# Kernel optimization log

Hardware: AMD Instinct MI355X
Metric: run time of the kernel (lower is better)

Reference implementation:

```python
import jax, jax.numpy as jnp
import numpy as np

N, E, EQ = 100000, 600000, 200000
F_IN, HID, N_CONVS = 128, 128, 4  # n_layers=3 -> 4 conv blocks
BN_EPS = 1e-5


def setup_inputs() -> dict:
    key = jax.random.key(0)
    ks = jax.random.split(key, 16)
    s = 1.0 / np.sqrt(HID)
    inp = {
        "x": jax.random.normal(ks[0], (N, F_IN), jnp.float32),
        "edge_index": jax.random.randint(ks[1], (2, E), 0, N, jnp.int64),
        "edge_attr": jax.random.uniform(ks[2], (E,), jnp.float32),
        "edge_label_index": jax.random.randint(ks[3], (2, EQ), 0, N, jnp.int64),
        # GraphConv params (layer 0 has in_dim == hidden_dim, so stack all 4)
        "rel_w": jax.random.normal(ks[4], (N_CONVS, HID, HID), jnp.float32) * s,
        "rel_b": jnp.zeros((N_CONVS, HID), jnp.float32),
        "root_w": jax.random.normal(ks[5], (N_CONVS, HID, HID), jnp.float32) * s,
        "bn_g": jnp.ones((N_CONVS, HID), jnp.float32),
        "bn_b": jnp.zeros((N_CONVS, HID), jnp.float32),
        # edge MLP: Linear(2H->H), GELU, Linear(H->1)
        "mlp_w1": jax.random.normal(ks[6], (2 * HID, HID), jnp.float32) * (1.0 / np.sqrt(2 * HID)),
        "mlp_b1": jnp.zeros((HID,), jnp.float32),
        "mlp_w2": jax.random.normal(ks[7], (HID, 1), jnp.float32) * s,
        "mlp_b2": jnp.zeros((1,), jnp.float32),
    }
    return inp


def reference(x, edge_index, edge_attr, edge_label_index,
              rel_w, rel_b, root_w, bn_g, bn_b,
              mlp_w1, mlp_b1, mlp_w2, mlp_b2):
    src, dst = edge_index[0], edge_index[1]
    n = x.shape[0]
    for l in range(rel_w.shape[0]):
        # GraphConv: lin_rel(sum_j w_ij * x_j) + lin_root(x_i)
        msg = x[src] * edge_attr[:, None]                      # [E, H] gather
        agg = jax.ops.segment_sum(msg, dst, num_segments=n)    # [N, H] scatter-add
        h = agg @ rel_w[l] + rel_b[l] + x @ root_w[l]
        h = jax.nn.gelu(h, approximate=False)
        # BatchNorm over nodes (training-mode batch stats, biased var)
        mean = h.mean(axis=0)
        var = h.var(axis=0)
        x = (h - mean) * jax.lax.rsqrt(var + BN_EPS) * bn_g[l] + bn_b[l]
    ef = jnp.concatenate([x[edge_label_index[0]], x[edge_label_index[1]]], axis=-1)  # [EQ, 2H]
    hmid = jax.nn.gelu(ef @ mlp_w1 + mlp_b1, approximate=False)
    out = jax.nn.sigmoid(hmid @ mlp_w2 + mlp_b2)
    return out.squeeze(-1)
```

## Files before the change

kernel.cpp:

```cpp
#include <hip/hip_runtime.h>

#define NN 100000
#define EE 600000
#define NQ 200000
#define HID 128
#define NL 4
#define BN_EPS 1e-5f
#define ECAP 1280

typedef __attribute__((ext_vector_type(8))) short short8;
typedef __attribute__((ext_vector_type(4))) float f32x4;

__device__ __forceinline__ float gelu_f(float v) {
    return 0.5f * v * (1.0f + erff(v * 0.70710678118654752f));
}
__device__ __forceinline__ unsigned short f2bf(float f) {
    unsigned int x = __float_as_uint(f);
    unsigned int r = (x + 0x7FFFu + ((x >> 16) & 1u)) >> 16;
    return (unsigned short)r;
}
__device__ __forceinline__ float bf2f(unsigned short u) {
    return __uint_as_float(((unsigned int)u) << 16);
}


__global__ void k_zero_int(int* __restrict__ p, int n) {
    int i = blockIdx.x * blockDim.x + threadIdx.x;
    if (i < n) p[i] = 0;
}

__global__ void k_cvt(const float* __restrict__ x, unsigned int* __restrict__ o, int n2) {
    int i = blockIdx.x * blockDim.x + threadIdx.x;
    if (i < n2) {
        float2 v = ((const float2*)x)[i];
        o[i] = (unsigned int)f2bf(v.x) | ((unsigned int)f2bf(v.y) << 16);
    }
}

__global__ void k_bninit(float* __restrict__ sc) {
    int i = threadIdx.x;
    sc[i] = (i < 128) ? 1.0f : 0.0f;
}


__global__ void k_hist(const int* __restrict__ ei, int* __restrict__ cnt) {
    int e = blockIdx.x * blockDim.x + threadIdx.x;
    if (e < EE) atomicAdd(&cnt[ei[EE + e]], 1);
}

__global__ void k_scan1(const int* __restrict__ cnt, int* __restrict__ rp,
                        int* __restrict__ bsum, int n) {
    __shared__ int sh[256];
    const int tid = threadIdx.x;
    const int base = blockIdx.x * 1024;
    int v[4];
    int s = 0;
    #pragma unroll
    for (int j = 0; j < 4; ++j) {
        int idx = base + tid * 4 + j;
        v[j] = (idx < n) ? cnt[idx] : 0;
        s += v[j];
    }
    sh[tid] = s;
    __syncthreads();
    for (int off = 1; off < 256; off <<= 1) {
        int t = (tid >= off) ? sh[tid - off] : 0;
        __syncthreads();
        sh[tid] += t;
        __syncthreads();
    }
    int run = sh[tid] - s;
    #pragma unroll
    for (int j = 0; j < 4; ++j) {
        int idx = base + tid * 4 + j;
        if (idx < n) rp[idx] = run;
        run += v[j];
    }
    if (tid == 255) bsum[blockIdx.x] = sh[255];
}

__global__ void k_scan2(int* __restrict__ bsum, int nb) {
    __shared__ int sh[256];
    const int tid = threadIdx.x;
    int v = (tid < nb) ? bsum[tid] : 0;
    sh[tid] = v;
    __syncthreads();
    for (int off = 1; off < 256; off <<= 1) {
        int t = (tid >= off) ? sh[tid - off] : 0;
        __syncthreads();
        sh[tid] += t;
        __syncthreads();
    }
    if (tid < nb) bsum[tid] = sh[tid] - v;
}

__global__ void k_scan3(int* __restrict__ rp, const int* __restrict__ bsum,
                        int* __restrict__ cnt, int n) {
    int i = blockIdx.x * blockDim.x + threadIdx.x;
    if (i < n) {
        rp[i] += bsum[i >> 10];
        cnt[i] = 0;
    }
    if (i == 0) rp[n] = EE;
}

__global__ void k_fill(const int* __restrict__ ei, const int* __restrict__ rp,
                       int* __restrict__ cur, int* __restrict__ eord) {
    int e = blockIdx.x * blockDim.x + threadIdx.x;
    if (e < EE) {
        int d = ei[EE + e];
        int p = rp[d] + atomicAdd(&cur[d], 1);
        eord[p] = e;
    }
}

__global__ void k_sortfill(const int* __restrict__ ei, const float* __restrict__ ea,
                           const int* __restrict__ rp, int* __restrict__ eord,
                           int* __restrict__ csrc, float* __restrict__ cea,
                           float* __restrict__ wdeg) {
    int n = blockIdx.x * blockDim.x + threadIdx.x;
    if (n >= NN) return;
    const int s0 = rp[n], s1 = rp[n + 1];
    for (int i = s0 + 1; i < s1; ++i) {
        int key = eord[i];
        int j = i - 1;
        while (j >= s0 && eord[j] > key) { eord[j + 1] = eord[j]; --j; }
        eord[j + 1] = key;
    }
    float s = 0.f;
    for (int i = s0; i < s1; ++i) {
        const int e = eord[i];
        csrc[i] = ei[e];
        const float w = ea[e];
        cea[i] = w;
        s += w;
    }
    wdeg[n] = s;
}


__global__ void k_wprep(const float* __restrict__ relw, const float* __restrict__ rootw,
                        const float* __restrict__ relb, const float* __restrict__ sc,
                        unsigned short* __restrict__ Wtf, float* __restrict__ bias2,
                        float* __restrict__ brel) {
    __shared__ float shb[256];
    const int n = blockIdx.x;
    const int k = threadIdx.x;
    const float s = sc[k & 127];
    const float w = (k < 128) ? relw[(size_t)k * HID + n] : rootw[(size_t)(k - 128) * HID + n];
    const int nb = n >> 4, l15 = n & 15;
    const int kc = k >> 5, kg = (k >> 3) & 3, e = k & 7;
    Wtf[((size_t)(kc * 8 + nb) * 512) + (kg * 16 + l15) * 8 + e] = f2bf(s * w);
    shb[k] = sc[128 + (k & 127)] * w;
    __syncthreads();
    #pragma unroll
    for (int off = 64; off >= 1; off >>= 1) {
        if (k < off) shb[k] += shb[k + off];
        else if (k >= 128 && k < 128 + off) shb[k] += shb[k + off];
        __syncthreads();
    }
    if (k == 0) brel[n] = shb[0];
    if (k == 128) bias2[n] = relb[n] + shb[128];
}

__global__ void k_mlpprep(const float* __restrict__ w1, const float* __restrict__ b1,
                          const float* __restrict__ sc, unsigned short* __restrict__ Wtm,
                          float* __restrict__ b1v) {
    __shared__ float shb[256];
    const int n = blockIdx.x;
    const int k = threadIdx.x;
    const float w = w1[(size_t)k * HID + n];
    Wtm[(size_t)n * 256 + k] = f2bf(sc[k & 127] * w);
    shb[k] = sc[128 + (k & 127)] * w;
    __syncthreads();
    #pragma unroll
    for (int off = 128; off >= 1; off >>= 1) {
        if (k < off) shb[k] += shb[k + off];
        __syncthreads();
    }
    if (k == 0) b1v[n] = b1[n] + shb[0];
}


__global__ __launch_bounds__(512, 6) void k_gemm2(
    const unsigned short* __restrict__ hprev, const int* __restrict__ csrc,
    const float* __restrict__ cea, const int* __restrict__ rp,
    const unsigned short* __restrict__ Wtf, const float* __restrict__ bias2,
    const float* __restrict__ brel, const float* __restrict__ wdeg,
    unsigned short* __restrict__ hnext, float* __restrict__ bnpart,
    int nrows, int nblk) {
    __shared__ unsigned short As[128 * 128];
    __shared__ float psb[8 * 64];
    __shared__ float pqb[8 * 64];
    __shared__ int eidx[ECAP];
    __shared__ float ew[ECAP];
    __shared__ int rps[132];
    const int tid = threadIdx.x;
    const int rb = blockIdx.x * 128;

    const int lane = tid & 63;
    const int wid = tid >> 6;
    const int wm = wid >> 1, wn = wid & 1;

    if (tid < 129) {
        int nn = rb + tid;
        rps[tid] = rp[nn < nrows ? nn : nrows];
    }
    __syncthreads();
    const int e0 = rps[0];
    const int ne = rps[128] - e0;
    const bool useLds = (ne <= ECAP);
    if (useLds) {
        for (int i = tid; i < ne; i += 512) {
            eidx[i] = csrc[e0 + i];
            ew[i] = cea[e0 + i];
        }
    }

    f32x4 acc[2][4];
    #pragma unroll
    for (int mf = 0; mf < 2; ++mf)
        #pragma unroll
        for (int nf = 0; nf < 4; ++nf) acc[mf][nf] = (f32x4){0.f, 0.f, 0.f, 0.f};

    #pragma unroll
    for (int s = 0; s < 2; ++s) {
        __syncthreads();
        if (s == 0) {
            const int g = lane >> 4;
            const int cl = lane & 15;
            for (int rr = 0; rr < 16; ++rr) {
                const int r = wid * 16 + rr;
                const int s0 = rps[r] - e0, s1 = rps[r + 1] - e0;
                float a0 = 0.f, a1 = 0.f, a2 = 0.f, a3 = 0.f,
                      a4 = 0.f, a5 = 0.f, a6 = 0.f, a7 = 0.f;
                for (int i = s0 + g; i < s1; i += 8) {
                    const int i2 = i + 4;
                    const bool has2 = i2 < s1;
                    int src1, src2;
                    float w1, w2;
                    if (useLds) {
                        src1 = eidx[i]; w1 = ew[i];
                        src2 = has2 ? eidx[i2] : src1;
                        w2 = has2 ? ew[i2] : 0.f;
                    } else {
                        src1 = csrc[e0 + i]; w1 = cea[e0 + i];
                        src2 = has2 ? csrc[e0 + i2] : src1;
                        w2 = has2 ? cea[e0 + i2] : 0.f;
                    }
                    const uint4 va = *(const uint4*)(hprev + (size_t)src1 * HID + cl * 8);
                    const uint4 vb = *(const uint4*)(hprev + (size_t)src2 * HID + cl * 8);
                    a0 += bf2f((unsigned short)(va.x)) * w1;
                    a1 += bf2f((unsigned short)(va.x >> 16)) * w1;
                    a2 += bf2f((unsigned short)(va.y)) * w1;
                    a3 += bf2f((unsigned short)(va.y >> 16)) * w1;
                    a4 += bf2f((unsigned short)(va.z)) * w1;
                    a5 += bf2f((unsigned short)(va.z >> 16)) * w1;
                    a6 += bf2f((unsigned short)(va.w)) * w1;
                    a7 += bf2f((unsigned short)(va.w >> 16)) * w1;
                    a0 += bf2f((unsigned short)(vb.x)) * w2;
                    a1 += bf2f((unsigned short)(vb.x >> 16)) * w2;
                    a2 += bf2f((unsigned short)(vb.y)) * w2;
                    a3 += bf2f((unsigned short)(vb.y >> 16)) * w2;
                    a4 += bf2f((unsigned short)(vb.z)) * w2;
                    a5 += bf2f((unsigned short)(vb.z >> 16)) * w2;
                    a6 += bf2f((unsigned short)(vb.w)) * w2;
                    a7 += bf2f((unsigned short)(vb.w >> 16)) * w2;
                }
                a0 += __shfl_xor(a0, 16); a1 += __shfl_xor(a1, 16);
                a2 += __shfl_xor(a2, 16); a3 += __shfl_xor(a3, 16);
                a4 += __shfl_xor(a4, 16); a5 += __shfl_xor(a5, 16);
                a6 += __shfl_xor(a6, 16); a7 += __shfl_xor(a7, 16);
                a0 += __shfl_xor(a0, 32); a1 += __shfl_xor(a1, 32);
                a2 += __shfl_xor(a2, 32); a3 += __shfl_xor(a3, 32);
                a4 += __shfl_xor(a4, 32); a5 += __shfl_xor(a5, 32);
                a6 += __shfl_xor(a6, 32); a7 += __shfl_xor(a7, 32);
                if (g == 0) {
                    uint4 o;
                    o.x = (unsigned int)f2bf(a0) | ((unsigned int)f2bf(a1) << 16);
                    o.y = (unsigned int)f2bf(a2) | ((unsigned int)f2bf(a3) << 16);
                    o.z = (unsigned int)f2bf(a4) | ((unsigned int)f2bf(a5) << 16);
                    o.w = (unsigned int)f2bf(a6) | ((unsigned int)f2bf(a7) << 16);
                    const int p = cl ^ (r & 7);
                    *(uint4*)(As + r * 128 + p * 8) = o;
                }
            }
        } else {
            #pragma unroll
            for (int i = 0; i < 4; ++i) {
                const int r = i * 32 + (tid >> 4);
                const int p = tid & 15;
                const int gr = min(rb + r, nrows - 1);
                const int gc = p ^ (r & 7);
                const uint4 v = *(const uint4*)(hprev + (size_t)gr * 128 + gc * 8);
                *(uint4*)(As + r * 128 + p * 8) = v;
            }
        }
        __syncthreads();
        #pragma unroll
        for (int kk = 0; kk < 4; ++kk) {
            short8 a[2], b[4];
            #pragma unroll
            for (int mf = 0; mf < 2; ++mf) {
                const int r = wm * 32 + mf * 16 + (lane & 15);
                const int p = (kk * 4 + (lane >> 4)) ^ (r & 7);
                a[mf] = *(const short8*)(As + r * 128 + p * 8);
            }
            #pragma unroll
            for (int nf = 0; nf < 4; ++nf) {
                b[nf] = *(const short8*)(Wtf + ((size_t)((s * 4 + kk) * 8 + wn * 4 + nf) * 512)
                                               + lane * 8);
            }
            #pragma unroll
            for (int mf = 0; mf < 2; ++mf)
                #pragma unroll
                for (int nf = 0; nf < 4; ++nf)
                    acc[mf][nf] = __builtin_amdgcn_mfma_f32_16x16x32_bf16(
                        a[mf], b[nf], acc[mf][nf], 0, 0, 0);
        }
    }

    int colv[4];
    float biasv[4], brelv[4];
    #pragma unroll
    for (int nf = 0; nf < 4; ++nf) {
        colv[nf] = wn * 64 + nf * 16 + (lane & 15);
        biasv[nf] = bias2[colv[nf]];
        brelv[nf] = brel[colv[nf]];
    }
    float ps[4] = {0.f, 0.f, 0.f, 0.f}, pq[4] = {0.f, 0.f, 0.f, 0.f};
    #pragma unroll
    for (int mf = 0; mf < 2; ++mf) {
        #pragma unroll
        for (int reg = 0; reg < 4; ++reg) {
            const int gm = rb + wm * 32 + mf * 16 + (lane >> 4) * 4 + reg;
            const bool valid = gm < nrows;
            const float wd = valid ? wdeg[gm] : 0.f;
            #pragma unroll
            for (int nf = 0; nf < 4; ++nf) {
                const float hv = gelu_f(acc[mf][nf][reg] + biasv[nf] + wd * brelv[nf]);
                if (valid) {
                    hnext[(size_t)gm * 128 + colv[nf]] = f2bf(hv);
                    ps[nf] += hv;
                    pq[nf] += hv * hv;
                }
            }
        }
    }
    #pragma unroll
    for (int nf = 0; nf < 4; ++nf) {
        ps[nf] += __shfl_xor(ps[nf], 16); ps[nf] += __shfl_xor(ps[nf], 32);
        pq[nf] += __shfl_xor(pq[nf], 16); pq[nf] += __shfl_xor(pq[nf], 32);
        if ((lane >> 4) == 0) {
            psb[wid * 64 + nf * 16 + (lane & 15)] = ps[nf];
            pqb[wid * 64 + nf * 16 + (lane & 15)] = pq[nf];
        }
    }
    __syncthreads();
    if (tid < 128) {
        const int wnh = tid >> 6;
        const int c64 = tid & 63;
        float s = 0.f, q = 0.f;
        #pragma unroll
        for (int w = 0; w < 4; ++w) {
            s += psb[(w * 2 + wnh) * 64 + c64];
            q += pqb[(w * 2 + wnh) * 64 + c64];
        }
        bnpart[(size_t)tid * nblk + blockIdx.x] = s;
        bnpart[(size_t)(128 + tid) * nblk + blockIdx.x] = q;
    }
}

__global__ void k_bnred(const float* __restrict__ bnpart, int nblk, float* __restrict__ bn) {
    __shared__ float sh[256];
    const int tid = threadIdx.x;
    const int col = blockIdx.x;
    float s = 0.f;
    for (int i = tid; i < nblk; i += 256) s += bnpart[(size_t)col * nblk + i];
    sh[tid] = s;
    __syncthreads();
    #pragma unroll
    for (int off = 128; off >= 1; off >>= 1) {
        if (tid < off) sh[tid] += sh[tid + off];
        __syncthreads();
    }
    if (tid == 0) bn[col] = sh[0];
}

__global__ void k_bnfin(const float* __restrict__ bn, const float* __restrict__ g,
                        const float* __restrict__ b, float* __restrict__ sc) {
    int i = threadIdx.x;
    if (i < 128) {
        const float inv_n = 1.0f / (float)NN;
        const float mean = bn[i] * inv_n;
        const float var = bn[128 + i] * inv_n - mean * mean;
        const float s = g[i] * rsqrtf(var + BN_EPS);
        sc[i] = s;
        sc[128 + i] = b[i] - mean * s;
    }
}


__global__ __launch_bounds__(512, 4) void k_mlp2(
    const unsigned short* __restrict__ xf, const int* __restrict__ eli,
    const unsigned short* __restrict__ Wtm, const float* __restrict__ b1v,
    const float* __restrict__ w2, const float* __restrict__ b2,
    float* __restrict__ out, int nq) {
    __shared__ unsigned short As[128 * 128];
    __shared__ unsigned short Bs[128 * 128];
    __shared__ int sidx[256];
    __shared__ float rowred2[2][128];
    const int tid = threadIdx.x;
    const int qb = blockIdx.x * 128;
    if (tid < 256) {
        const int rr = tid & 127;
        const int q = qb + rr;
        sidx[tid] = (q < nq) ? eli[(tid >> 7) * NQ + q] : 0;
    }
    __syncthreads();

    const int lane = tid & 63;
    const int wid = tid >> 6;
    const int wm = wid >> 1, wn = wid & 1;

    f32x4 acc[2][4];
    #pragma unroll
    for (int mf = 0; mf < 2; ++mf)
        #pragma unroll
        for (int nf = 0; nf < 4; ++nf) acc[mf][nf] = (f32x4){0.f, 0.f, 0.f, 0.f};

    #pragma unroll
    for (int s = 0; s < 2; ++s) {
        if (s) __syncthreads();
        #pragma unroll
        for (int i = 0; i < 4; ++i) {
            const int r = i * 32 + (tid >> 4);
            const int p = tid & 15;
            const int node = sidx[s * 128 + r];
            const int gc = p ^ (r & 7);
            const uint4 v = *(const uint4*)(xf + (size_t)node * 128 + gc * 8);
            *(uint4*)(As + r * 128 + p * 8) = v;
        }
        #pragma unroll
        for (int i = 0; i < 4; ++i) {
            const int n = i * 32 + (tid >> 4);
            const int p = tid & 15;
            const int gc = s * 16 + (p ^ (n & 7));
            const uint4 v = *(const uint4*)(Wtm + (size_t)n * 256 + gc * 8);
            *(uint4*)(Bs + n * 128 + p * 8) = v;
        }
        __syncthreads();
        #pragma unroll
        for (int kk = 0; kk < 4; ++kk) {
            short8 a[2], b[4];
            #pragma unroll
            for (int mf = 0; mf < 2; ++mf) {
                const int r = wm * 32 + mf * 16 + (lane & 15);
                const int p = (kk * 4 + (lane >> 4)) ^ (r & 7);
                a[mf] = *(const short8*)(As + r * 128 + p * 8);
            }
            #pragma unroll
            for (int nf = 0; nf < 4; ++nf) {
                const int n = wn * 64 + nf * 16 + (lane & 15);
                const int p = (kk * 4 + (lane >> 4)) ^ (n & 7);
                b[nf] = *(const short8*)(Bs + n * 128 + p * 8);
            }
            #pragma unroll
            for (int mf = 0; mf < 2; ++mf)
                #pragma unroll
                for (int nf = 0; nf < 4; ++nf)
                    acc[mf][nf] = __builtin_amdgcn_mfma_f32_16x16x32_bf16(
                        a[mf], b[nf], acc[mf][nf], 0, 0, 0);
        }
    }

    int colv[4];
    float w2v[4], b1c[4];
    #pragma unroll
    for (int nf = 0; nf < 4; ++nf) {
        colv[nf] = wn * 64 + nf * 16 + (lane & 15);
        w2v[nf] = w2[colv[nf]];
        b1c[nf] = b1v[colv[nf]];
    }
    #pragma unroll
    for (int mf = 0; mf < 2; ++mf) {
        #pragma unroll
        for (int reg = 0; reg < 4; ++reg) {
            float part = 0.f;
            #pragma unroll
            for (int nf = 0; nf < 4; ++nf)
                part += gelu_f(acc[mf][nf][reg] + b1c[nf]) * w2v[nf];
            part += __shfl_xor(part, 1);
            part += __shfl_xor(part, 2);
            part += __shfl_xor(part, 4);
            part += __shfl_xor(part, 8);
            if ((lane & 15) == 0) {
                const int lr = wm * 32 + mf * 16 + (lane >> 4) * 4 + reg;
                rowred2[wn][lr] = part;
            }
        }
    }
    __syncthreads();
    if (tid < 128) {
        const int q = qb + tid;
        if (q < nq)
            out[q] = 1.0f / (1.0f + expf(-(rowred2[0][tid] + rowred2[1][tid] + b2[0])));
    }
}


extern "C" void kernel_launch(void* const* d_in, const int* in_sizes, int n_in,
                              void* d_out, int out_size, void* d_ws, size_t ws_size,
                              hipStream_t stream) {
    const float* x_in = (const float*)d_in[0];
    const int* ei = (const int*)d_in[1];
    const float* ea = (const float*)d_in[2];
    const int* eli = (const int*)d_in[3];
    const float* rel_w = (const float*)d_in[4];
    const float* rel_b = (const float*)d_in[5];
    const float* root_w = (const float*)d_in[6];
    const float* bn_g = (const float*)d_in[7];
    const float* bn_b = (const float*)d_in[8];
    const float* w1 = (const float*)d_in[9];
    const float* b1 = (const float*)d_in[10];
    const float* w2 = (const float*)d_in[11];
    const float* b2 = (const float*)d_in[12];
    float* out = (float*)d_out;

    char* ws = (char*)d_ws;
    size_t off = 0;
    auto alloc = [&](size_t bytes) -> void* {
        void* p = ws + off;
        off = (off + bytes + 255) & ~(size_t)255;
        return p;
    };
    const int nblk_gemm = (NN + 127) / 128;
    unsigned short* hb0 = (unsigned short*)alloc(2ull * NN * HID);
    unsigned short* hb1 = (unsigned short*)alloc(2ull * NN * HID);
    int* eord = (int*)alloc(sizeof(int) * EE);
    int* csrc = (int*)alloc(sizeof(int) * EE);
    float* cea = (float*)alloc(sizeof(float) * EE);
    int* rp = (int*)alloc(sizeof(int) * (NN + 1));
    int* cnt = (int*)alloc(sizeof(int) * NN);
    int* bsum = (int*)alloc(sizeof(int) * 256);
    float* wdeg = (float*)alloc(sizeof(float) * NN);
    float* bnpart = (float*)alloc(sizeof(float) * 256 * (size_t)nblk_gemm);
    float* bn = (float*)alloc(sizeof(float) * 256);
    float* bnsc = (float*)alloc(sizeof(float) * 256);
    unsigned short* Wtf = (unsigned short*)alloc(2ull * 128 * 256);
    unsigned short* Wtm = (unsigned short*)alloc(2ull * 128 * 256);
    float* bias2 = (float*)alloc(sizeof(float) * 128);
    float* brel = (float*)alloc(sizeof(float) * 128);
    float* b1v = (float*)alloc(sizeof(float) * 128);
    (void)ws_size;

    const int nb_scan = (NN + 1023) / 1024;

    k_cvt<<<(NN * 64 + 255) / 256, 256, 0, stream>>>(x_in, (unsigned int*)hb0, NN * 64);

    k_zero_int<<<(NN + 255) / 256, 256, 0, stream>>>(cnt, NN);
    k_hist<<<(EE + 255) / 256, 256, 0, stream>>>(ei, cnt);
    k_scan1<<<nb_scan, 256, 0, stream>>>(cnt, rp, bsum, NN);
    k_scan2<<<1, 256, 0, stream>>>(bsum, nb_scan);
    k_scan3<<<(NN + 255) / 256, 256, 0, stream>>>(rp, bsum, cnt, NN);
    k_fill<<<(EE + 255) / 256, 256, 0, stream>>>(ei, rp, cnt, eord);
    k_sortfill<<<(NN + 255) / 256, 256, 0, stream>>>(ei, ea, rp, eord, csrc, cea, wdeg);
    k_bninit<<<1, 256, 0, stream>>>(bnsc);

    unsigned short* hcur = hb0;
    unsigned short* bufs[2] = {hb1, hb0};
    for (int l = 0; l < NL; ++l) {
        unsigned short* hnext = bufs[l & 1];
        k_wprep<<<128, 256, 0, stream>>>(rel_w + (size_t)l * HID * HID,
                                         root_w + (size_t)l * HID * HID,
                                         rel_b + (size_t)l * HID, bnsc, Wtf, bias2, brel);
        k_gemm2<<<nblk_gemm, 512, 0, stream>>>(hcur, csrc, cea, rp, Wtf, bias2, brel, wdeg,
                                               hnext, bnpart, NN, nblk_gemm);
        k_bnred<<<256, 256, 0, stream>>>(bnpart, nblk_gemm, bn);
        k_bnfin<<<1, 128, 0, stream>>>(bn, bn_g + (size_t)l * HID, bn_b + (size_t)l * HID, bnsc);
        hcur = hnext;
    }

    k_mlpprep<<<128, 256, 0, stream>>>(w1, b1, bnsc, Wtm, b1v);
    k_mlp2<<<(NQ + 127) / 128, 512, 0, stream>>>(hcur, eli, Wtm, b1v, w2, b2, out, NQ);
}
```

Measured before the change: 457.7 us.

## Stage GEMM output through LDS, fuse BN reduce/finalize, read MLP weights pre-fragmented

The layer GEMM now writes its GELU output to shared memory and then stores whole rows to global memory with 16-byte vector stores, replacing scattered 2-byte stores. The BN partial reduction and the finalize step are merged into one kernel, removing one launch per layer. The edge-MLP weights are laid out in MFMA fragment order so k_mlp2 reads B operands straight from global/L2, which drops the Bs shared buffer and lets launch bounds rise to 6 blocks. The costs are an extra barrier in the GEMM and B operands that now come from L2 instead of LDS.

After: 461.1 us. About the same (+0.8%).

```diff
diff --git a/kernel.cpp b/kernel.cpp
--- a/kernel.cpp
+++ b/kernel.cpp
@@ -164,13 +164,15 @@
 }
 
 __global__ void k_mlpprep(const float* __restrict__ w1, const float* __restrict__ b1,
-                          const float* __restrict__ sc, unsigned short* __restrict__ Wtm,
+                          const float* __restrict__ sc, unsigned short* __restrict__ Wtmf,
                           float* __restrict__ b1v) {
     __shared__ float shb[256];
     const int n = blockIdx.x;
     const int k = threadIdx.x;
     const float w = w1[(size_t)k * HID + n];
-    Wtm[(size_t)n * 256 + k] = f2bf(sc[k & 127] * w);
+    const int nb = n >> 4, l15 = n & 15;
+    const int kc = k >> 5, kg = (k >> 3) & 3, e = k & 7;
+    Wtmf[((size_t)(kc * 8 + nb) * 512) + (kg * 16 + l15) * 8 + e] = f2bf(sc[k & 127] * w);
     shb[k] = sc[128 + (k & 127)] * w;
     __syncthreads();
     #pragma unroll
@@ -320,6 +322,8 @@
         }
     }
 
+    __syncthreads();
+
     int colv[4];
     float biasv[4], brelv[4];
     #pragma unroll
@@ -333,14 +337,15 @@
     for (int mf = 0; mf < 2; ++mf) {
         #pragma unroll
         for (int reg = 0; reg < 4; ++reg) {
-            const int gm = rb + wm * 32 + mf * 16 + (lane >> 4) * 4 + reg;
+            const int lr = wm * 32 + mf * 16 + (lane >> 4) * 4 + reg;
+            const int gm = rb + lr;
             const bool valid = gm < nrows;
             const float wd = valid ? wdeg[gm] : 0.f;
             #pragma unroll
             for (int nf = 0; nf < 4; ++nf) {
                 const float hv = gelu_f(acc[mf][nf][reg] + biasv[nf] + wd * brelv[nf]);
+                As[lr * 128 + colv[nf]] = f2bf(hv);
                 if (valid) {
-                    hnext[(size_t)gm * 128 + colv[nf]] = f2bf(hv);
                     ps[nf] += hv;
                     pq[nf] += hv * hv;
                 }
@@ -357,6 +362,16 @@
         }
     }
     __syncthreads();
+
+    const int nvalid = nrows - rb;
+    #pragma unroll
+    for (int it = 0; it < 4; ++it) {
+        const int r = it * 32 + (tid >> 4);
+        const int c16 = tid & 15;
+        if (r < nvalid)
+            *(uint4*)(hnext + (size_t)(rb + r) * 128 + c16 * 8) =
+                *(const uint4*)(As + r * 128 + c16 * 8);
+    }
     if (tid < 128) {
         const int wnh = tid >> 6;
         const int c64 = tid & 63;
@@ -371,43 +386,43 @@
     }
 }
 
-__global__ void k_bnred(const float* __restrict__ bnpart, int nblk, float* __restrict__ bn) {
+__global__ void k_bnredfin(const float* __restrict__ bnpart, int nblk,
+                           const float* __restrict__ g, const float* __restrict__ b,
+                           float* __restrict__ sc) {
     __shared__ float sh[256];
+    __shared__ float sh2[256];
     const int tid = threadIdx.x;
     const int col = blockIdx.x;
-    float s = 0.f;
-    for (int i = tid; i < nblk; i += 256) s += bnpart[(size_t)col * nblk + i];
+    float s = 0.f, q = 0.f;
+    for (int i = tid; i < nblk; i += 256) {
+        s += bnpart[(size_t)col * nblk + i];
+        q += bnpart[(size_t)(128 + col) * nblk + i];
+    }
     sh[tid] = s;
+    sh2[tid] = q;
     __syncthreads();
     #pragma unroll
     for (int off = 128; off >= 1; off >>= 1) {
-        if (tid < off) sh[tid] += sh[tid + off];
-        __syncthreads();
-    }
-    if (tid == 0) bn[col] = sh[0];
-}
-
-__global__ void k_bnfin(const float* __restrict__ bn, const float* __restrict__ g,
-                        const float* __restrict__ b, float* __restrict__ sc) {
-    int i = threadIdx.x;
-    if (i < 128) {
+        if (tid < off) { sh[tid] += sh[tid + off]; sh2[tid] += sh2[tid + off]; }
+        __syncthreads();
+    }
+    if (tid == 0) {
         const float inv_n = 1.0f / (float)NN;
-        const float mean = bn[i] * inv_n;
-        const float var = bn[128 + i] * inv_n - mean * mean;
-        const float s = g[i] * rsqrtf(var + BN_EPS);
-        sc[i] = s;
-        sc[128 + i] = b[i] - mean * s;
-    }
-}
-
-
-__global__ __launch_bounds__(512, 4) void k_mlp2(
+        const float mean = sh[0] * inv_n;
+        const float var = sh2[0] * inv_n - mean * mean;
+        const float scale = g[col] * rsqrtf(var + BN_EPS);
+        sc[col] = scale;
+        sc[128 + col] = b[col] - mean * scale;
+    }
+}
+
+
+__global__ __launch_bounds__(512, 6) void k_mlp2(
     const unsigned short* __restrict__ xf, const int* __restrict__ eli,
-    const unsigned short* __restrict__ Wtm, const float* __restrict__ b1v,
+    const unsigned short* __restrict__ Wtmf, const float* __restrict__ b1v,
     const float* __restrict__ w2, const float* __restrict__ b2,
     float* __restrict__ out, int nq) {
     __shared__ unsigned short As[128 * 128];
-    __shared__ unsigned short Bs[128 * 128];
     __shared__ int sidx[256];
     __shared__ float rowred2[2][128];
     const int tid = threadIdx.x;
@@ -441,14 +456,6 @@
             const uint4 v = *(const uint4*)(xf + (size_t)node * 128 + gc * 8);
             *(uint4*)(As + r * 128 + p * 8) = v;
         }
-        #pragma unroll
-        for (int i = 0; i < 4; ++i) {
-            const int n = i * 32 + (tid >> 4);
-            const int p = tid & 15;
-            const int gc = s * 16 + (p ^ (n & 7));
-            const uint4 v = *(const uint4*)(Wtm + (size_t)n * 256 + gc * 8);
-            *(uint4*)(Bs + n * 128 + p * 8) = v;
-        }
         __syncthreads();
         #pragma unroll
         for (int kk = 0; kk < 4; ++kk) {
@@ -461,9 +468,8 @@
             }
             #pragma unroll
             for (int nf = 0; nf < 4; ++nf) {
-                const int n = wn * 64 + nf * 16 + (lane & 15);
-                const int p = (kk * 4 + (lane >> 4)) ^ (n & 7);
-                b[nf] = *(const short8*)(Bs + n * 128 + p * 8);
+                b[nf] = *(const short8*)(Wtmf + ((size_t)((s * 4 + kk) * 8 + wn * 4 + nf) * 512)
+                                               + lane * 8);
             }
             #pragma unroll
             for (int mf = 0; mf < 2; ++mf)
@@ -545,10 +551,9 @@
     int* bsum = (int*)alloc(sizeof(int) * 256);
     float* wdeg = (float*)alloc(sizeof(float) * NN);
     float* bnpart = (float*)alloc(sizeof(float) * 256 * (size_t)nblk_gemm);
-    float* bn = (float*)alloc(sizeof(float) * 256);
     float* bnsc = (float*)alloc(sizeof(float) * 256);
     unsigned short* Wtf = (unsigned short*)alloc(2ull * 128 * 256);
-    unsigned short* Wtm = (unsigned short*)alloc(2ull * 128 * 256);
+    unsigned short* Wtmf = (unsigned short*)alloc(2ull * 128 * 256);
     float* bias2 = (float*)alloc(sizeof(float) * 128);
     float* brel = (float*)alloc(sizeof(float) * 128);
     float* b1v = (float*)alloc(sizeof(float) * 128);
@@ -576,11 +581,11 @@
                                          rel_b + (size_t)l * HID, bnsc, Wtf, bias2, brel);
         k_gemm2<<<nblk_gemm, 512, 0, stream>>>(hcur, csrc, cea, rp, Wtf, bias2, brel, wdeg,
                                                hnext, bnpart, NN, nblk_gemm);
-        k_bnred<<<256, 256, 0, stream>>>(bnpart, nblk_gemm, bn);
-        k_bnfin<<<1, 128, 0, stream>>>(bn, bn_g + (size_t)l * HID, bn_b + (size_t)l * HID, bnsc);
+        k_bnredfin<<<128, 256, 0, stream>>>(bnpart, nblk_gemm,
+                                            bn_g + (size_t)l * HID, bn_b + (size_t)l * HID, bnsc);
         hcur = hnext;
     }
 
-    k_mlpprep<<<128, 256, 0, stream>>>(w1, b1, bnsc, Wtm, b1v);
-    k_mlp2<<<(NQ + 127) / 128, 512, 0, stream>>>(hcur, eli, Wtm, b1v, w2, b2, out, NQ);
-}
+    k_mlpprep<<<128, 256, 0, stream>>>(w1, b1, bnsc, Wtmf, b1v);
+    k_mlp2<<<(NQ + 127) / 128, 512, 0, stream>>>(hcur, eli, Wtmf, b1v, w2, b2, out, NQ);
+}
```
